# Kernel tuning notes

Measured on AMD Instinct MI355X. Metric: run time of the kernel, lower is better.

The kernel has to match this reference:

```python
import jax, jax.numpy as jnp
import numpy as np

ALPHA = 0.2       # LeakyReLU negative slope
LN_EPS = 1e-5     # nn.LayerNorm default eps
MASK_VAL = -1e9   # masked_fill value in original


def setup_inputs() -> dict:
    key = jax.random.key(0)
    ks = jax.random.split(key, 8)
    B, N, D_IN, D_OUT = 1, 1024, 64, 64
    def lin(k, fan_in, shape):
        return jax.random.normal(k, shape, dtype=jnp.float32) / np.sqrt(fan_in)
    return {
        "h": jax.random.normal(ks[0], (B, N, D_IN), dtype=jnp.float32),
        "adj": jax.random.randint(ks[1], (B, N, N), 0, 2, dtype=jnp.int32),
        "W": lin(ks[2], D_IN, (D_IN, D_OUT)),                 # W (no bias)
        "attn_w1": lin(ks[3], 3 * D_OUT, (3 * D_OUT, D_OUT)),  # attention_mlp layer 1
        "attn_b1": jnp.zeros((D_OUT,), jnp.float32),
        "attn_w2": lin(ks[4], D_OUT, (D_OUT, 1)),              # attention_mlp layer 2
        "attn_b2": jnp.zeros((1,), jnp.float32),
        "edge_w": lin(ks[5], 2 * D_IN, (2 * D_IN, D_OUT)),     # edge_encoder linear
        "edge_b": jnp.zeros((D_OUT,), jnp.float32),
        "ln_g": jnp.ones((D_OUT,), jnp.float32),
        "ln_b": jnp.zeros((D_OUT,), jnp.float32),
    }


def reference(h, adj, W, attn_w1, attn_b1, attn_w2, attn_b2, edge_w, edge_b, ln_g, ln_b):
    # Eval mode: dropout is identity. in_features == out_features -> residual_proj is None.
    d_in = h.shape[-1]
    d = W.shape[1]
    Wh = h @ W  # [b, n, d]

    # Split concat-linears into per-block matmuls (math identical to cat+Linear,
    # avoids materializing the [b,n,n,3d] and [b,n,n,2d] concat tensors).
    E_i, E_j = edge_w[:d_in], edge_w[d_in:]
    ei = h @ E_i  # [b, n, d]
    ej = h @ E_j
    # edge_encoder(cat(h_i, h_j)) -> [b, n, n, d]
    edge = jax.nn.leaky_relu(ei[:, :, None, :] + ej[:, None, :, :] + edge_b, ALPHA)

    A_i, A_j, A_e = attn_w1[:d], attn_w1[d:2 * d], attn_w1[2 * d:]
    pre = ((Wh @ A_i)[:, :, None, :] + (Wh @ A_j)[:, None, :, :]
           + edge @ A_e + attn_b1)                      # [b, n, n, d]
    hid = jax.nn.leaky_relu(pre, ALPHA)
    e = jnp.squeeze(hid @ attn_w2, -1) + attn_b2[0]     # [b, n, n]

    e = jnp.where(adj == 0, MASK_VAL, e)
    attention = jax.nn.softmax(e, axis=-1)              # [b, n, n]

    h_prime = attention @ Wh + h                        # residual (in == out)

    mu = jnp.mean(h_prime, axis=-1, keepdims=True)
    var = jnp.mean(jnp.square(h_prime - mu), axis=-1, keepdims=True)
    out = (h_prime - mu) / jnp.sqrt(var + LN_EPS) * ln_g + ln_b
    return out
```

## Files before the change

### kernel.cpp

```cpp
#include <hip/hip_runtime.h>
#include <math.h>

#define N 1024
#define D 64
#define ALPHA 0.2f
#define LN_EPS 1e-5f
#define MASK_VAL -1000000000.0f

typedef __attribute__((ext_vector_type(8))) short bf16x8;
typedef __attribute__((ext_vector_type(4))) float f32x4;
typedef __attribute__((ext_vector_type(2))) float f32x2;

__device__ __forceinline__ unsigned f2bf_u(float f) {
    unsigned u = __builtin_bit_cast(unsigned, f);
    u += 0x7fffu + ((u >> 16) & 1u);
    return u >> 16;
}
__device__ __forceinline__ short f2bf(float f) { return (short)f2bf_u(f); }

__device__ __forceinline__ unsigned rne_pair(float x, float y) {
    unsigned ux = __builtin_bit_cast(unsigned, x);
    unsigned uy = __builtin_bit_cast(unsigned, y);
    ux += 0x7fffu + ((ux >> 16) & 1u);
    uy += 0x7fffu + ((uy >> 16) & 1u);
    return __builtin_amdgcn_perm(uy, ux, 0x07060302);
}

__device__ __forceinline__ f32x4 leaky4(f32x4 v) {
    return __builtin_elementwise_max(v, v * 0.2f);
}

union BF8 { bf16x8 v; unsigned u[4]; };

__global__ __launch_bounds__(256) void gat_precompute(
    const float* __restrict__ h, const float* __restrict__ W,
    const float* __restrict__ attn_w1, const float* __restrict__ attn_b1,
    const float* __restrict__ edge_w, const float* __restrict__ edge_b,
    float* __restrict__ Wh, float* __restrict__ ejB, float* __restrict__ aj,
    float* __restrict__ ei, float* __restrict__ aiB)
{
    const int tid = threadIdx.x;
    const int r = tid >> 6;
    const int k = tid & 63;
    const int i = blockIdx.x * 4 + r;
    __shared__ float hrow[4][D];
    __shared__ float whrow[4][D];

    hrow[r][k] = h[(size_t)i * D + k];
    __syncthreads();

    float wh = 0.f, vei = 0.f, vej = 0.f;
    #pragma unroll 8
    for (int m = 0; m < D; ++m) {
        float hm = hrow[r][m];
        wh  = fmaf(hm, W[m * D + k], wh);
        vei = fmaf(hm, edge_w[m * D + k], vei);
        vej = fmaf(hm, edge_w[(m + D) * D + k], vej);
    }
    Wh[(size_t)i * D + k]  = wh;
    ei[(size_t)i * D + k]  = vei;
    ejB[(size_t)i * D + k] = vej + edge_b[k];
    whrow[r][k] = wh;
    __syncthreads();

    float vai = 0.f, vaj = 0.f;
    #pragma unroll 8
    for (int m = 0; m < D; ++m) {
        float wm = whrow[r][m];
        vai = fmaf(wm, attn_w1[m * D + k], vai);
        vaj = fmaf(wm, attn_w1[(m + D) * D + k], vaj);
    }
    aiB[(size_t)i * D + k] = vai + attn_b1[k];
    aj[(size_t)i * D + k]  = vaj;
}

__global__ __launch_bounds__(256) void gat_scores(
    const float* __restrict__ ejB, const float* __restrict__ aj,
    const float* __restrict__ ei, const float* __restrict__ aiB,
    const float* __restrict__ attn_w1, const float* __restrict__ attn_w2,
    const float* __restrict__ attn_b2, const int* __restrict__ adj,
    float* __restrict__ e_out)
{
    const int tid  = threadIdx.x;
    const int lane = tid & 63;
    const int wid  = tid >> 6;
    const int nloc = lane & 15;
    const int quad = lane >> 4;
    const int i0   = (blockIdx.x >> 2) * 4;
    const int jb   = (blockIdx.x & 3) * 256 + wid * 64;
    const float* __restrict__ Ae = attn_w1 + 128 * D;

    __shared__ __align__(16) float sv[4][D];
    __shared__ __align__(16) float av[4][D];

    sv[tid >> 6][tid & 63] = ei[(size_t)(i0 + (tid >> 6)) * D + (tid & 63)];
    av[tid >> 6][tid & 63] = aiB[(size_t)(i0 + (tid >> 6)) * D + (tid & 63)];
    __syncthreads();

    bf16x8 Bf[2][4];
    #pragma unroll
    for (int kt = 0; kt < 2; ++kt)
        #pragma unroll
        for (int ot = 0; ot < 4; ++ot)
            #pragma unroll
            for (int idx = 0; idx < 8; ++idx) {
                int k = kt * 32 + quad * 8 + idx;
                Bf[kt][ot][idx] = f2bf(Ae[(size_t)k * D + ot * 16 + nloc]);
            }

    f32x4 w2l[4];
    #pragma unroll
    for (int ot = 0; ot < 4; ++ot)
        w2l[ot] = *(const f32x4*)(attn_w2 + ot * 16 + quad * 4);
    const float b2 = attn_b2[0];
    const int k0 = quad * 8;

    for (int jt = 0; jt < 4; ++jt) {
        const int j16 = jb + jt * 16;
        const int jrow = j16 + nloc;
        const float* __restrict__ ejr = ejB + (size_t)jrow * D;
        const float* __restrict__ ajr = aj + (size_t)jrow * D;

        f32x4 ev0 = *(const f32x4*)(ejr + k0);
        f32x4 ev1 = *(const f32x4*)(ejr + k0 + 4);
        f32x4 ev2 = *(const f32x4*)(ejr + 32 + k0);
        f32x4 ev3 = *(const f32x4*)(ejr + 32 + k0 + 4);
        f32x4 ajv[4];
        #pragma unroll
        for (int ot = 0; ot < 4; ++ot)
            ajv[ot] = *(const f32x4*)(ajr + ot * 16 + quad * 4);

        #pragma unroll
        for (int ii = 0; ii < 4; ++ii) {
            const f32x4 s0 = *(const f32x4*)(&sv[ii][k0]);
            const f32x4 s1 = *(const f32x4*)(&sv[ii][k0 + 4]);
            const f32x4 s2 = *(const f32x4*)(&sv[ii][32 + k0]);
            const f32x4 s3 = *(const f32x4*)(&sv[ii][32 + k0 + 4]);

            BF8 af0, af1;
            f32x4 t;
            t = leaky4(ev0 + s0); af0.u[0] = rne_pair(t.x, t.y); af0.u[1] = rne_pair(t.z, t.w);
            t = leaky4(ev1 + s1); af0.u[2] = rne_pair(t.x, t.y); af0.u[3] = rne_pair(t.z, t.w);
            t = leaky4(ev2 + s2); af1.u[0] = rne_pair(t.x, t.y); af1.u[1] = rne_pair(t.z, t.w);
            t = leaky4(ev3 + s3); af1.u[2] = rne_pair(t.x, t.y); af1.u[3] = rne_pair(t.z, t.w);

            f32x4 acc[4];
            #pragma unroll
            for (int ot = 0; ot < 4; ++ot) {
                f32x4 avl = *(const f32x4*)(&av[ii][ot * 16 + quad * 4]);
                acc[ot] = __builtin_amdgcn_mfma_f32_16x16x32_bf16(Bf[0][ot], af0.v, ajv[ot] + avl, 0, 0, 0);
                acc[ot] = __builtin_amdgcn_mfma_f32_16x16x32_bf16(Bf[1][ot], af1.v, acc[ot], 0, 0, 0);
            }

            f32x2 e2 = {0.f, 0.f};
            #pragma unroll
            for (int ot = 0; ot < 4; ++ot) {
                f32x4 hd = leaky4(acc[ot]);
                e2 += hd.lo * w2l[ot].lo;
                e2 += hd.hi * w2l[ot].hi;
            }
            float e = e2.x + e2.y;
            e += __shfl_xor(e, 16, 64);
            e += __shfl_xor(e, 32, 64);

            if (lane < 16) {
                const int j = j16 + lane;
                const size_t idx = (size_t)(i0 + ii) * N + j;
                const int a = adj[idx];
                e_out[idx] = a ? (e + b2) : MASK_VAL;
            }
        }
    }
}

__global__ __launch_bounds__(256) void gat_softagg(
    const float* __restrict__ e_in, const float* __restrict__ Wh,
    const float* __restrict__ h, const float* __restrict__ ln_g,
    const float* __restrict__ ln_b, float* __restrict__ out)
{
    const int tid  = threadIdx.x;
    const int lane = tid & 63;
    const int wid  = tid >> 6;
    const int i0   = blockIdx.x * 2;
    const int r    = wid >> 1;
    const int half = wid & 1;

    __shared__ float p[2][N];
    __shared__ float wred[4][2];
    __shared__ float red[4][2][D];

    {
        const float* __restrict__ erow = e_in + (size_t)(i0 + r) * N;
        float m = -INFINITY;
        #pragma unroll
        for (int c = 0; c < 8; ++c) {
            int j = half * 512 + c * 64 + lane;
            float v = erow[j];
            p[r][j] = v;
            m = fmaxf(m, v);
        }
        #pragma unroll
        for (int off = 32; off >= 1; off >>= 1) m = fmaxf(m, __shfl_xor(m, off, 64));
        if (lane == 0) wred[wid][0] = m;
    }
    __syncthreads();
    {
        float m = fmaxf(wred[r * 2][0], wred[r * 2 + 1][0]);
        float s = 0.f;
        #pragma unroll
        for (int c = 0; c < 8; ++c) {
            int j = half * 512 + c * 64 + lane;
            float pv = __expf(p[r][j] - m);
            p[r][j] = pv;
            s += pv;
        }
        #pragma unroll
        for (int off = 32; off >= 1; off >>= 1) s += __shfl_xor(s, off, 64);
        if (lane == 0) wred[wid][1] = s;
    }
    __syncthreads();

    {
        const int k = lane, g = wid;
        float hp0 = 0.f, hp1 = 0.f;
        #pragma unroll 8
        for (int jj = 0; jj < 256; ++jj) {
            const int j = g * 256 + jj;
            const float whv = Wh[(size_t)j * D + k];
            hp0 = fmaf(p[0][j], whv, hp0);
            hp1 = fmaf(p[1][j], whv, hp1);
        }
        red[g][0][k] = hp0;
        red[g][1][k] = hp1;
    }
    __syncthreads();

    if (wid < 2) {
        const int rr = wid;
        const float inv_s = 1.f / (wred[rr * 2][1] + wred[rr * 2 + 1][1]);
        float v = (red[0][rr][lane] + red[1][rr][lane] +
                   red[2][rr][lane] + red[3][rr][lane]) * inv_s
                  + h[(size_t)(i0 + rr) * D + lane];
        float mu = v;
        #pragma unroll
        for (int off = 32; off >= 1; off >>= 1) mu += __shfl_xor(mu, off, 64);
        mu *= (1.f / D);
        float d = v - mu;
        float var = d * d;
        #pragma unroll
        for (int off = 32; off >= 1; off >>= 1) var += __shfl_xor(var, off, 64);
        var *= (1.f / D);
        out[(size_t)(i0 + rr) * D + lane] = d * rsqrtf(var + LN_EPS) * ln_g[lane] + ln_b[lane];
    }
}

extern "C" void kernel_launch(void* const* d_in, const int* in_sizes, int n_in,
                              void* d_out, int out_size, void* d_ws, size_t ws_size,
                              hipStream_t stream) {
    const float* h       = (const float*)d_in[0];
    const int*   adj     = (const int*)  d_in[1];
    const float* W       = (const float*)d_in[2];
    const float* attn_w1 = (const float*)d_in[3];
    const float* attn_b1 = (const float*)d_in[4];
    const float* attn_w2 = (const float*)d_in[5];
    const float* attn_b2 = (const float*)d_in[6];
    const float* edge_w  = (const float*)d_in[7];
    const float* edge_b  = (const float*)d_in[8];
    const float* ln_g    = (const float*)d_in[9];
    const float* ln_b    = (const float*)d_in[10];
    float* out = (float*)d_out;

    float* ws  = (float*)d_ws;
    float* Wh  = ws + 0 * (N * D);
    float* ejB = ws + 1 * (N * D);
    float* aj  = ws + 2 * (N * D);
    float* ei  = ws + 3 * (N * D);
    float* aiB = ws + 4 * (N * D);
    float* e   = ws + 5 * (N * D);

    gat_precompute<<<N / 4, 256, 0, stream>>>(h, W, attn_w1, attn_b1, edge_w, edge_b,
                                              Wh, ejB, aj, ei, aiB);
    gat_scores<<<(N / 4) * 4, 256, 0, stream>>>(ejB, aj, ei, aiB,
                                                attn_w1, attn_w2, attn_b2, adj, e);
    gat_softagg<<<N / 2, 256, 0, stream>>>(e, Wh, h, ln_g, ln_b, out);
}
```

Before: 149.5 us.

## Rewrite edge leaky-ReLU as linear plus abs term, retile score kernel

Uses leaky(x) = 0.6x + 0.4|x| so the linear part of edge@A_e is folded into the per-node aj/ai precompute, leaving only an abs() (a sign-bit mask) before the bf16 MFMA on the n×n path. The score kernel is retiled so each block handles 16 query rows against 64 columns. The MFMA operands are swapped so the output layout lets the w2 reduction run through lane shuffles and the adjacency read and score write become vectorized int4/float4 accesses. aj is stored transposed to match. This trims the per-pair VALU work and improves reuse, at the cost of more precompute and different rounding, since the 0.4 factor is now applied to bf16 weights.

Result: faster. 127.2 us (-15.0%).

```diff
diff --git a/kernel.cpp b/kernel.cpp
--- a/kernel.cpp
+++ b/kernel.cpp
@@ -9,7 +9,8 @@
 
 typedef __attribute__((ext_vector_type(8))) short bf16x8;
 typedef __attribute__((ext_vector_type(4))) float f32x4;
-typedef __attribute__((ext_vector_type(2))) float f32x2;
+
+__device__ __forceinline__ float leaky(float x) { return fmaxf(x, ALPHA * x); }
 
 __device__ __forceinline__ unsigned f2bf_u(float f) {
     unsigned u = __builtin_bit_cast(unsigned, f);
@@ -18,16 +19,12 @@
 }
 __device__ __forceinline__ short f2bf(float f) { return (short)f2bf_u(f); }
 
-__device__ __forceinline__ unsigned rne_pair(float x, float y) {
-    unsigned ux = __builtin_bit_cast(unsigned, x);
-    unsigned uy = __builtin_bit_cast(unsigned, y);
+__device__ __forceinline__ unsigned abs_rne_pair(float x, float y) {
+    unsigned ux = __builtin_bit_cast(unsigned, x) & 0x7fffffffu;
+    unsigned uy = __builtin_bit_cast(unsigned, y) & 0x7fffffffu;
     ux += 0x7fffu + ((ux >> 16) & 1u);
     uy += 0x7fffu + ((uy >> 16) & 1u);
     return __builtin_amdgcn_perm(uy, ux, 0x07060302);
-}
-
-__device__ __forceinline__ f32x4 leaky4(f32x4 v) {
-    return __builtin_elementwise_max(v, v * 0.2f);
 }
 
 union BF8 { bf16x8 v; unsigned u[4]; };
@@ -36,15 +33,15 @@
     const float* __restrict__ h, const float* __restrict__ W,
     const float* __restrict__ attn_w1, const float* __restrict__ attn_b1,
     const float* __restrict__ edge_w, const float* __restrict__ edge_b,
-    float* __restrict__ Wh, float* __restrict__ ejB, float* __restrict__ aj,
-    float* __restrict__ ei, float* __restrict__ aiB)
+    float* __restrict__ Wh, float* __restrict__ ejB, float* __restrict__ ei_o,
+    float* __restrict__ ajT, float* __restrict__ aiF)
 {
     const int tid = threadIdx.x;
     const int r = tid >> 6;
     const int k = tid & 63;
     const int i = blockIdx.x * 4 + r;
-    __shared__ float hrow[4][D];
-    __shared__ float whrow[4][D];
+    const float* __restrict__ Ae = attn_w1 + 2 * D * D;
+    __shared__ float hrow[4][D], whrow[4][D], eirow[4][D], ejrow[4][D];
 
     hrow[r][k] = h[(size_t)i * D + k];
     __syncthreads();
@@ -57,26 +54,30 @@
         vei = fmaf(hm, edge_w[m * D + k], vei);
         vej = fmaf(hm, edge_w[(m + D) * D + k], vej);
     }
-    Wh[(size_t)i * D + k]  = wh;
-    ei[(size_t)i * D + k]  = vei;
-    ejB[(size_t)i * D + k] = vej + edge_b[k];
-    whrow[r][k] = wh;
-    __syncthreads();
-
-    float vai = 0.f, vaj = 0.f;
+    vej += edge_b[k];
+    Wh[(size_t)i * D + k]   = wh;
+    ei_o[(size_t)i * D + k] = vei;
+    ejB[(size_t)i * D + k]  = vej;
+    whrow[r][k] = wh; eirow[r][k] = vei; ejrow[r][k] = vej;
+    __syncthreads();
+
+    float vai = 0.f, vaj = 0.f, vea = 0.f, veb = 0.f;
     #pragma unroll 8
     for (int m = 0; m < D; ++m) {
         float wm = whrow[r][m];
+        float aem = Ae[m * D + k];
         vai = fmaf(wm, attn_w1[m * D + k], vai);
         vaj = fmaf(wm, attn_w1[(m + D) * D + k], vaj);
-    }
-    aiB[(size_t)i * D + k] = vai + attn_b1[k];
-    aj[(size_t)i * D + k]  = vaj;
+        vea = fmaf(ejrow[r][m], aem, vea);
+        veb = fmaf(eirow[r][m], aem, veb);
+    }
+    ajT[(size_t)k * N + i]  = vaj + 0.6f * vea;
+    aiF[(size_t)i * D + k]  = vai + attn_b1[k] + 0.6f * veb;
 }
 
 __global__ __launch_bounds__(256) void gat_scores(
-    const float* __restrict__ ejB, const float* __restrict__ aj,
-    const float* __restrict__ ei, const float* __restrict__ aiB,
+    const float* __restrict__ ejB, const float* __restrict__ ajT,
+    const float* __restrict__ ei, const float* __restrict__ aiF,
     const float* __restrict__ attn_w1, const float* __restrict__ attn_w2,
     const float* __restrict__ attn_b2, const int* __restrict__ adj,
     float* __restrict__ e_out)
@@ -86,15 +87,21 @@
     const int wid  = tid >> 6;
     const int nloc = lane & 15;
     const int quad = lane >> 4;
-    const int i0   = (blockIdx.x >> 2) * 4;
-    const int jb   = (blockIdx.x & 3) * 256 + wid * 64;
-    const float* __restrict__ Ae = attn_w1 + 128 * D;
-
-    __shared__ __align__(16) float sv[4][D];
-    __shared__ __align__(16) float av[4][D];
-
-    sv[tid >> 6][tid & 63] = ei[(size_t)(i0 + (tid >> 6)) * D + (tid & 63)];
-    av[tid >> 6][tid & 63] = aiB[(size_t)(i0 + (tid >> 6)) * D + (tid & 63)];
+    const int i0   = (blockIdx.x >> 4) * 16;
+    const int j16  = (blockIdx.x & 15) * 64 + wid * 16;
+    const float* __restrict__ Ae = attn_w1 + 2 * D * D;
+
+    __shared__ __align__(16) float sv[16][D];
+    __shared__ float av[16][D];
+    {
+        float* svf = &sv[0][0];
+        float* avf = &av[0][0];
+        #pragma unroll
+        for (int c = 0; c < 4; ++c) {
+            svf[c * 256 + tid] = ei[(size_t)i0 * D + c * 256 + tid];
+            avf[c * 256 + tid] = aiF[(size_t)i0 * D + c * 256 + tid];
+        }
+    }
     __syncthreads();
 
     bf16x8 Bf[2][4];
@@ -105,70 +112,73 @@
             #pragma unroll
             for (int idx = 0; idx < 8; ++idx) {
                 int k = kt * 32 + quad * 8 + idx;
-                Bf[kt][ot][idx] = f2bf(Ae[(size_t)k * D + ot * 16 + nloc]);
+                Bf[kt][ot][idx] = f2bf(0.4f * Ae[(size_t)k * D + ot * 16 + nloc]);
             }
 
-    f32x4 w2l[4];
+    float w2l[4];
+    #pragma unroll
+    for (int ot = 0; ot < 4; ++ot) w2l[ot] = attn_w2[ot * 16 + nloc];
+    const float b2 = attn_b2[0];
+    const int k0 = quad * 8;
+
+    const float* __restrict__ ejr = ejB + (size_t)(j16 + nloc) * D;
+    const f32x4 ev0 = *(const f32x4*)(ejr + k0);
+    const f32x4 ev1 = *(const f32x4*)(ejr + k0 + 4);
+    const f32x4 ev2 = *(const f32x4*)(ejr + 32 + k0);
+    const f32x4 ev3 = *(const f32x4*)(ejr + 32 + k0 + 4);
+    f32x4 ajv[4];
     #pragma unroll
     for (int ot = 0; ot < 4; ++ot)
-        w2l[ot] = *(const f32x4*)(attn_w2 + ot * 16 + quad * 4);
-    const float b2 = attn_b2[0];
-    const int k0 = quad * 8;
-
-    for (int jt = 0; jt < 4; ++jt) {
-        const int j16 = jb + jt * 16;
-        const int jrow = j16 + nloc;
-        const float* __restrict__ ejr = ejB + (size_t)jrow * D;
-        const float* __restrict__ ajr = aj + (size_t)jrow * D;
-
-        f32x4 ev0 = *(const f32x4*)(ejr + k0);
-        f32x4 ev1 = *(const f32x4*)(ejr + k0 + 4);
-        f32x4 ev2 = *(const f32x4*)(ejr + 32 + k0);
-        f32x4 ev3 = *(const f32x4*)(ejr + 32 + k0 + 4);
-        f32x4 ajv[4];
-        #pragma unroll
-        for (int ot = 0; ot < 4; ++ot)
-            ajv[ot] = *(const f32x4*)(ajr + ot * 16 + quad * 4);
-
-        #pragma unroll
-        for (int ii = 0; ii < 4; ++ii) {
-            const f32x4 s0 = *(const f32x4*)(&sv[ii][k0]);
-            const f32x4 s1 = *(const f32x4*)(&sv[ii][k0 + 4]);
-            const f32x4 s2 = *(const f32x4*)(&sv[ii][32 + k0]);
-            const f32x4 s3 = *(const f32x4*)(&sv[ii][32 + k0 + 4]);
-
-            BF8 af0, af1;
-            f32x4 t;
-            t = leaky4(ev0 + s0); af0.u[0] = rne_pair(t.x, t.y); af0.u[1] = rne_pair(t.z, t.w);
-            t = leaky4(ev1 + s1); af0.u[2] = rne_pair(t.x, t.y); af0.u[3] = rne_pair(t.z, t.w);
-            t = leaky4(ev2 + s2); af1.u[0] = rne_pair(t.x, t.y); af1.u[1] = rne_pair(t.z, t.w);
-            t = leaky4(ev3 + s3); af1.u[2] = rne_pair(t.x, t.y); af1.u[3] = rne_pair(t.z, t.w);
-
-            f32x4 acc[4];
+        ajv[ot] = *(const f32x4*)(ajT + (size_t)(ot * 16 + nloc) * N + j16 + quad * 4);
+
+    #pragma unroll 4
+    for (int ii = 0; ii < 16; ++ii) {
+        const f32x4 s0 = *(const f32x4*)(&sv[ii][k0]);
+        const f32x4 s1 = *(const f32x4*)(&sv[ii][k0 + 4]);
+        const f32x4 s2 = *(const f32x4*)(&sv[ii][32 + k0]);
+        const f32x4 s3 = *(const f32x4*)(&sv[ii][32 + k0 + 4]);
+
+        BF8 af0, af1;
+        f32x4 t;
+        t = ev0 + s0; af0.u[0] = abs_rne_pair(t.x, t.y); af0.u[1] = abs_rne_pair(t.z, t.w);
+        t = ev1 + s1; af0.u[2] = abs_rne_pair(t.x, t.y); af0.u[3] = abs_rne_pair(t.z, t.w);
+        t = ev2 + s2; af1.u[0] = abs_rne_pair(t.x, t.y); af1.u[1] = abs_rne_pair(t.z, t.w);
+        t = ev3 + s3; af1.u[2] = abs_rne_pair(t.x, t.y); af1.u[3] = abs_rne_pair(t.z, t.w);
+
+        f32x4 acc[4];
+        #pragma unroll
+        for (int ot = 0; ot < 4; ++ot) {
+            acc[ot] = __builtin_amdgcn_mfma_f32_16x16x32_bf16(af0.v, Bf[0][ot], ajv[ot], 0, 0, 0);
+            acc[ot] = __builtin_amdgcn_mfma_f32_16x16x32_bf16(af1.v, Bf[1][ot], acc[ot], 0, 0, 0);
+        }
+
+        float part[4] = {0.f, 0.f, 0.f, 0.f};
+        #pragma unroll
+        for (int ot = 0; ot < 4; ++ot) {
+            const float avli = av[ii][ot * 16 + nloc];
             #pragma unroll
-            for (int ot = 0; ot < 4; ++ot) {
-                f32x4 avl = *(const f32x4*)(&av[ii][ot * 16 + quad * 4]);
-                acc[ot] = __builtin_amdgcn_mfma_f32_16x16x32_bf16(Bf[0][ot], af0.v, ajv[ot] + avl, 0, 0, 0);
-                acc[ot] = __builtin_amdgcn_mfma_f32_16x16x32_bf16(Bf[1][ot], af1.v, acc[ot], 0, 0, 0);
-            }
-
-            f32x2 e2 = {0.f, 0.f};
-            #pragma unroll
-            for (int ot = 0; ot < 4; ++ot) {
-                f32x4 hd = leaky4(acc[ot]);
-                e2 += hd.lo * w2l[ot].lo;
-                e2 += hd.hi * w2l[ot].hi;
-            }
-            float e = e2.x + e2.y;
-            e += __shfl_xor(e, 16, 64);
-            e += __shfl_xor(e, 32, 64);
-
-            if (lane < 16) {
-                const int j = j16 + lane;
-                const size_t idx = (size_t)(i0 + ii) * N + j;
-                const int a = adj[idx];
-                e_out[idx] = a ? (e + b2) : MASK_VAL;
-            }
+            for (int r = 0; r < 4; ++r)
+                part[r] = fmaf(leaky(acc[ot][r] + avli), w2l[ot], part[r]);
+        }
+        #pragma unroll
+        for (int r = 0; r < 4; ++r) {
+            float v = part[r];
+            v += __shfl_xor(v, 1, 64);
+            v += __shfl_xor(v, 2, 64);
+            v += __shfl_xor(v, 4, 64);
+            v += __shfl_xor(v, 8, 64);
+            part[r] = v;
+        }
+        if (nloc == 0) {
+            const int jr = j16 + quad * 4;
+            const size_t base = (size_t)(i0 + ii) * N + jr;
+            const int4 am = *(const int4*)(adj + base);
+            f32x4 res;
+            res.x = am.x ? part[0] + b2 : MASK_VAL;
+            res.y = am.y ? part[1] + b2 : MASK_VAL;
+            res.z = am.z ? part[2] + b2 : MASK_VAL;
+            res.w = am.w ? part[3] + b2 : MASK_VAL;
+            *(f32x4*)(e_out + base) = res;
         }
     }
 }
@@ -270,17 +280,17 @@
     const float* ln_b    = (const float*)d_in[10];
     float* out = (float*)d_out;
 
-    float* ws  = (float*)d_ws;
-    float* Wh  = ws + 0 * (N * D);
-    float* ejB = ws + 1 * (N * D);
-    float* aj  = ws + 2 * (N * D);
-    float* ei  = ws + 3 * (N * D);
-    float* aiB = ws + 4 * (N * D);
-    float* e   = ws + 5 * (N * D);
+    float* ws   = (float*)d_ws;
+    float* Wh   = ws + 0 * (N * D);
+    float* ejB  = ws + 1 * (N * D);
+    float* ei_w = ws + 2 * (N * D);
+    float* ajT  = ws + 3 * (N * D);
+    float* aiF  = ws + 4 * (N * D);
+    float* e    = ws + 5 * (N * D);
 
     gat_precompute<<<N / 4, 256, 0, stream>>>(h, W, attn_w1, attn_b1, edge_w, edge_b,
-                                              Wh, ejB, aj, ei, aiB);
-    gat_scores<<<(N / 4) * 4, 256, 0, stream>>>(ejB, aj, ei, aiB,
-                                                attn_w1, attn_w2, attn_b2, adj, e);
+                                              Wh, ejB, ei_w, ajT, aiF);
+    gat_scores<<<(N / 16) * 16, 256, 0, stream>>>(ejB, ajT, ei_w, aiF,
+                                                  attn_w1, attn_w2, attn_b2, adj, e);
     gat_softagg<<<N / 2, 256, 0, stream>>>(e, Wh, h, ln_g, ln_b, out);
 }
```
